# Performance work log

Measured on AMD Instinct MI355X. Metric: run time of the kernel, lower is better.

## Reference

```python
import jax, jax.numpy as jnp
import numpy as np

N = 100000   # nodes
E = 1600000  # edges (avg degree 16)
F = 128      # num_features
H = 128      # hidden_channels
C = 8        # num_classes


def _gcn_conv(x, src, dst, W, b, num_nodes):
    """PyG GCNConv: add self-loops, symmetric normalization, linear-then-aggregate, +bias."""
    h = x @ W  # [N, out]
    loops = jnp.arange(num_nodes, dtype=src.dtype)
    s = jnp.concatenate([src, loops])
    d = jnp.concatenate([dst, loops])
    deg = jax.ops.segment_sum(jnp.ones_like(s, dtype=h.dtype), d, num_segments=num_nodes)
    dinv = jax.lax.rsqrt(jnp.maximum(deg, 1.0))  # deg >= 1 thanks to self-loops
    norm = dinv[s] * dinv[d]  # [E+N]
    out = jax.ops.segment_sum(h[s] * norm[:, None], d, num_segments=num_nodes)
    return out + b


def setup_inputs() -> dict:
    key = jax.random.key(0)
    k1, k2, k3, k4 = jax.random.split(key, 4)
    x = jax.random.normal(k1, (N, F), dtype=jnp.float32)
    edge_index = jax.random.randint(k2, (2, E), 0, N, dtype=jnp.int32)
    W1 = jax.random.normal(k3, (F, H), dtype=jnp.float32) * (1.0 / np.sqrt(F))
    b1 = jnp.zeros((H,), dtype=jnp.float32)
    W2 = jax.random.normal(k4, (H, C), dtype=jnp.float32) * (1.0 / np.sqrt(H))
    b2 = jnp.zeros((C,), dtype=jnp.float32)
    return {"x": x, "edge_index": edge_index, "W1": W1, "b1": b1, "W2": W2, "b2": b2}


def reference(x, edge_index, W1, b1, W2, b2):
    src, dst = edge_index[0], edge_index[1]
    h = _gcn_conv(x, src, dst, W1, b1, N)
    h = jax.nn.relu(h)
    out = _gcn_conv(h, src, dst, W2, b2, N)
    return out
```

## Files before the change

kernel.cpp:

```cpp
#include <hip/hip_runtime.h>
#include <hip/hip_bf16.h>
#include <hip/hip_fp16.h>

#define NN 100000
#define EE 1600000
#define FF 128
#define HH 128
#define CC 8

#define CH 8192
#define NBK ((NN + 255) / 256)
#define NCH ((EE + CH - 1) / CH)
#define HSZ (NBK * NCH)
#define NT ((NN + 63) / 64)
#define G1B 320

typedef _Float16 half8 __attribute__((ext_vector_type(8)));
typedef float f32x4 __attribute__((ext_vector_type(4)));

__global__ __launch_bounds__(1024) void k_scan1(const int* __restrict__ in,
                                                int* __restrict__ outp,
                                                int* __restrict__ bsum, int n) {
  __shared__ int sh[1024];
  int t = threadIdx.x;
  int i = blockIdx.x * 1024 + t;
  int v = (i < n) ? in[i] : 0;
  sh[t] = v;
  __syncthreads();
  for (int offs = 1; offs < 1024; offs <<= 1) {
    int add = (t >= offs) ? sh[t - offs] : 0;
    __syncthreads();
    sh[t] += add;
    __syncthreads();
  }
  if (i < n) outp[i] = sh[t] - v;
  if (t == 1023) bsum[blockIdx.x] = sh[1023];
}

__global__ __launch_bounds__(256) void k_scan2(int* __restrict__ bsum, int nb) {
  __shared__ int sh[256];
  int t = threadIdx.x;
  int v = (t < nb) ? bsum[t] : 0;
  sh[t] = v;
  __syncthreads();
  for (int offs = 1; offs < 256; offs <<= 1) {
    int add = (t >= offs) ? sh[t - offs] : 0;
    __syncthreads();
    sh[t] += add;
    __syncthreads();
  }
  if (t < nb) bsum[t] = sh[t] - v;
}

__global__ __launch_bounds__(256) void k_histA(const int* __restrict__ dst,
                                               int* __restrict__ hist) {
  __shared__ int lh[NBK];
  int c = blockIdx.x, t = threadIdx.x;
  for (int b = t; b < NBK; b += 256) lh[b] = 0;
  __syncthreads();
  int e0 = c * CH, e1 = min(e0 + CH, EE);
  for (int j = e0 + t; j < e1; j += 256) atomicAdd(&lh[dst[j] >> 8], 1);
  __syncthreads();
  for (int b = t; b < NBK; b += 256) hist[b * NCH + c] = lh[b];
}

__global__ __launch_bounds__(256) void k_scat_gemm1(
    const int* __restrict__ src, const int* __restrict__ dst,
    const int* __restrict__ hist_s, const int* __restrict__ bsum,
    unsigned int* __restrict__ stage,
    const float* __restrict__ x, const float* __restrict__ W,
    __half* __restrict__ h, int n) {
  __shared__ _Float16 Wl[128 * 128];
  int t = threadIdx.x;

  if (blockIdx.x < NCH) {
    int* lcur = (int*)Wl;
    int c = blockIdx.x;
    for (int b = t; b < NBK; b += 256) {
      int idx = b * NCH + c;
      lcur[b] = hist_s[idx] + bsum[idx >> 10];
    }
    __syncthreads();
    int e0 = c * CH, e1 = min(e0 + CH, EE);
    for (int j = e0 + t; j < e1; j += 256) {
      int d = dst[j];
      int pos = atomicAdd(&lcur[d >> 8], 1);
      stage[pos] = (unsigned int)src[j] | ((unsigned int)(d & 255) << 17);
    }
    return;
  }

  {
    int c = t & 127;
    int kg0 = t >> 7;
    for (int kg = kg0; kg < 16; kg += 2) {
      _Float16 tmp[8];
#pragma unroll
      for (int j = 0; j < 8; ++j)
        tmp[j] = (_Float16)W[(size_t)(kg * 8 + j) * 128 + c];
      int byteoff = (c * 256 + kg * 16) ^ ((c & 7) << 4);
      *(half8*)((char*)Wl + byteoff) = *(half8*)tmp;
    }
  }
  __syncthreads();

  int w = t >> 6, l = t & 63;
  int rw = w >> 1, cw = w & 1;
  int lr = l & 15, g = l >> 4;

  for (int tile = blockIdx.x - NCH; tile < NT; tile += G1B) {
    int row0 = tile * 64;
    f32x4 acc[2][4];
#pragma unroll
    for (int ar = 0; ar < 2; ++ar)
#pragma unroll
      for (int bt = 0; bt < 4; ++bt)
#pragma unroll
        for (int r = 0; r < 4; ++r) acc[ar][bt][r] = 0.f;

    for (int kt = 0; kt < 4; ++kt) {
      half8 a[2];
#pragma unroll
      for (int ar = 0; ar < 2; ++ar) {
        int row = row0 + rw * 32 + ar * 16 + lr;
        if (row < n) {
          const float* p = &x[(size_t)row * 128 + kt * 32 + g * 8];
          float4 v0 = *(const float4*)p;
          float4 v1 = *(const float4*)(p + 4);
          a[ar][0] = (_Float16)v0.x; a[ar][1] = (_Float16)v0.y;
          a[ar][2] = (_Float16)v0.z; a[ar][3] = (_Float16)v0.w;
          a[ar][4] = (_Float16)v1.x; a[ar][5] = (_Float16)v1.y;
          a[ar][6] = (_Float16)v1.z; a[ar][7] = (_Float16)v1.w;
        } else {
#pragma unroll
          for (int j = 0; j < 8; ++j) a[ar][j] = (_Float16)0.f;
        }
      }
#pragma unroll
      for (int bt = 0; bt < 4; ++bt) {
        int c = cw * 64 + bt * 16 + lr;
        int byteoff = (c * 256 + kt * 64 + g * 16) ^ ((c & 7) << 4);
        half8 bb = *(const half8*)((const char*)Wl + byteoff);
        acc[0][bt] = __builtin_amdgcn_mfma_f32_16x16x32_f16(a[0], bb, acc[0][bt], 0, 0, 0);
        acc[1][bt] = __builtin_amdgcn_mfma_f32_16x16x32_f16(a[1], bb, acc[1][bt], 0, 0, 0);
      }
    }

#pragma unroll
    for (int ar = 0; ar < 2; ++ar)
#pragma unroll
      for (int bt = 0; bt < 4; ++bt)
#pragma unroll
        for (int r = 0; r < 4; ++r) {
          int row = row0 + rw * 32 + ar * 16 + g * 4 + r;
          int c = cw * 64 + bt * 16 + lr;
          if (row < n) h[(size_t)row * 128 + c] = __float2half(acc[ar][bt][r]);
        }
  }
}

__global__ __launch_bounds__(256) void k_bucketB(const unsigned int* __restrict__ stage,
                                                 const int* __restrict__ hist_s,
                                                 const int* __restrict__ bsum,
                                                 int* __restrict__ col,
                                                 int* __restrict__ rowptr,
                                                 float* __restrict__ dinv) {
  __shared__ int lcnt[256];
  __shared__ int lpart[256];
  int b = blockIdx.x, t = threadIdx.x;
  int n0 = b * 256;
  lcnt[t] = 0;
  int i0 = b * NCH;
  int e0 = hist_s[i0] + bsum[i0 >> 10];
  int e1;
  if (b == NBK - 1) {
    e1 = EE;
  } else {
    int i1 = (b + 1) * NCH;
    e1 = hist_s[i1] + bsum[i1 >> 10];
  }
  __syncthreads();
  for (int j = e0 + t; j < e1; j += 256)
    atomicAdd(&lcnt[stage[j] >> 17], 1);
  __syncthreads();
  int c = lcnt[t];
  lpart[t] = c;
  __syncthreads();
  for (int offs = 1; offs < 256; offs <<= 1) {
    int add = (t >= offs) ? lpart[t - offs] : 0;
    __syncthreads();
    lpart[t] += add;
    __syncthreads();
  }
  int base = e0 + lpart[t] - c;
  int node = n0 + t;
  if (node <= NN) rowptr[node] = base;
  if (node < NN) dinv[node] = rsqrtf((float)c + 1.f);
  __syncthreads();
  lcnt[t] = base;
  __syncthreads();
  for (int j = e0 + t; j < e1; j += 256) {
    unsigned int v = stage[j];
    int pos = atomicAdd(&lcnt[v >> 17], 1);
    col[pos] = (int)(v & 0x1FFFFu);
  }
}

__global__ __launch_bounds__(256) void k_agg1(const __half* __restrict__ h,
                                              const int* __restrict__ rowptr,
                                              const int* __restrict__ col,
                                              const float* __restrict__ dinv,
                                              const float* __restrict__ b1,
                                              __half2* __restrict__ out, int n) {
  int wid = threadIdx.x >> 6;
  int lane = threadIdx.x & 63;
  int node = blockIdx.x * 4 + wid;
  if (node >= n) return;
  float dn = dinv[node];
  const __half2* hp = (const __half2*)h;
  float2 acc = make_float2(0.f, 0.f);
  int e0 = rowptr[node], e1 = rowptr[node + 1];
  int e = e0;
  for (; e + 7 < e1; e += 8) {
    int s[8];
#pragma unroll
    for (int u = 0; u < 8; ++u) s[u] = col[e + u];
    float w[8];
    __half2 f[8];
#pragma unroll
    for (int u = 0; u < 8; ++u) w[u] = dinv[s[u]];
#pragma unroll
    for (int u = 0; u < 8; ++u) f[u] = hp[(size_t)s[u] * 64 + lane];
#pragma unroll
    for (int u = 0; u < 8; ++u) {
      float2 ff = __half22float2(f[u]);
      float ww = w[u] * dn;
      acc.x = fmaf(ww, ff.x, acc.x);
      acc.y = fmaf(ww, ff.y, acc.y);
    }
  }
  for (; e + 1 < e1; e += 2) {
    int s0 = col[e], s1 = col[e + 1];
    float w0 = dinv[s0] * dn, w1 = dinv[s1] * dn;
    float2 f0 = __half22float2(hp[(size_t)s0 * 64 + lane]);
    float2 f1 = __half22float2(hp[(size_t)s1 * 64 + lane]);
    acc.x = fmaf(w0, f0.x, acc.x); acc.y = fmaf(w0, f0.y, acc.y);
    acc.x = fmaf(w1, f1.x, acc.x); acc.y = fmaf(w1, f1.y, acc.y);
  }
  if (e < e1) {
    int s = col[e];
    float w = dinv[s] * dn;
    float2 f = __half22float2(hp[(size_t)s * 64 + lane]);
    acc.x = fmaf(w, f.x, acc.x);
    acc.y = fmaf(w, f.y, acc.y);
  }
  {
    float w = dn * dn;
    float2 f = __half22float2(hp[(size_t)node * 64 + lane]);
    acc.x = fmaf(w, f.x, acc.x);
    acc.y = fmaf(w, f.y, acc.y);
  }
  float2 bb = ((const float2*)b1)[lane];
  acc.x = fmaxf(acc.x + bb.x, 0.f);
  acc.y = fmaxf(acc.y + bb.y, 0.f);
  out[(size_t)node * 64 + lane] = __floats2half2_rn(acc.x, acc.y);
}

__global__ __launch_bounds__(256) void k_gemm2(const __half* __restrict__ a,
                                               const float* __restrict__ W2,
                                               __half* __restrict__ h2, int n) {
  int r = blockIdx.x * 256 + threadIdx.x;
  if (r >= n) return;
  float acc[8];
#pragma unroll
  for (int c = 0; c < 8; ++c) acc[c] = 0.f;
  const __half2* ap = (const __half2*)(a + (size_t)r * 128);
#pragma unroll 8
  for (int k2 = 0; k2 < 64; ++k2) {
    float2 v = __half22float2(ap[k2]);
    int k = k2 * 2;
#pragma unroll
    for (int c = 0; c < 8; ++c) {
      acc[c] = fmaf(v.x, W2[(k + 0) * 8 + c], acc[c]);
      acc[c] = fmaf(v.y, W2[(k + 1) * 8 + c], acc[c]);
    }
  }
  union { __half2 h2v[4]; uint4 u; } pk;
#pragma unroll
  for (int c = 0; c < 4; ++c)
    pk.h2v[c] = __floats2half2_rn(acc[2 * c], acc[2 * c + 1]);
  *(uint4*)&h2[(size_t)r * 8] = pk.u;
}

__global__ __launch_bounds__(256) void k_agg2(const __half* __restrict__ h2,
                                              const int* __restrict__ rowptr,
                                              const int* __restrict__ col,
                                              const float* __restrict__ dinv,
                                              const float* __restrict__ b2,
                                              float* __restrict__ out, int n) {
  int gthread = blockIdx.x * 256 + threadIdx.x;
  int node = gthread >> 3, f = gthread & 7;
  if (node >= n) return;
  float dn = dinv[node];
  float acc = 0.f;
  int e0 = rowptr[node], e1 = rowptr[node + 1];
  int e = e0;
  for (; e + 7 < e1; e += 8) {
    int s[8];
#pragma unroll
    for (int u = 0; u < 8; ++u) s[u] = col[e + u];
    float w[8];
    float v[8];
#pragma unroll
    for (int u = 0; u < 8; ++u) w[u] = dinv[s[u]];
#pragma unroll
    for (int u = 0; u < 8; ++u) v[u] = __half2float(h2[(size_t)s[u] * 8 + f]);
#pragma unroll
    for (int u = 0; u < 8; ++u) acc = fmaf(w[u] * dn, v[u], acc);
  }
  for (; e < e1; ++e) {
    int s = col[e];
    acc = fmaf(dinv[s] * dn, __half2float(h2[(size_t)s * 8 + f]), acc);
  }
  acc = fmaf(dn * dn, __half2float(h2[(size_t)node * 8 + f]), acc);
  out[(size_t)node * 8 + f] = acc + b2[f];
}

extern "C" void kernel_launch(void* const* d_in, const int* in_sizes, int n_in,
                              void* d_out, int out_size, void* d_ws, size_t ws_size,
                              hipStream_t stream) {
  const float* x  = (const float*)d_in[0];
  const int* eidx = (const int*)d_in[1];
  const float* W1 = (const float*)d_in[2];
  const float* b1 = (const float*)d_in[3];
  const float* W2 = (const float*)d_in[4];
  const float* b2 = (const float*)d_in[5];
  float* out = (float*)d_out;
  const int* src = eidx;
  const int* dst = eidx + EE;

  char* ws = (char*)d_ws;
  size_t off = 0;
  auto alloc = [&](size_t bytes) -> char* {
    char* p = ws + off;
    off = (off + bytes + 255) & ~(size_t)255;
    return p;
  };

  float*        dinv   = (float*)       alloc((size_t)NN * 4);
  int*          rowptr = (int*)         alloc((size_t)(NN + 1) * 4);
  int*          bsum   = (int*)         alloc(1024 * 4);
  int*          hist_g = (int*)         alloc((size_t)HSZ * 4);
  int*          hist_s = (int*)         alloc((size_t)HSZ * 4);
  unsigned int* stage  = (unsigned int*)alloc((size_t)EE * 4);
  int*          colbuf = (int*)         alloc((size_t)EE * 4);
  __half*       h1     = (__half*)      alloc((size_t)NN * HH * 2);
  __half2*      agg1   = (__half2*)     alloc((size_t)NN * HH * 2);
  __half*       h2     = (__half*)h1;

  int nbScanH = (HSZ + 1023) / 1024;

  k_histA<<<NCH, 256, 0, stream>>>(dst, hist_g);
  k_scan1<<<nbScanH, 1024, 0, stream>>>(hist_g, hist_s, bsum, HSZ);
  k_scan2<<<1, 256, 0, stream>>>(bsum, nbScanH);

  k_scat_gemm1<<<NCH + G1B, 256, 0, stream>>>(src, dst, hist_s, bsum, stage,
                                              x, W1, h1, NN);
  k_bucketB<<<NBK, 256, 0, stream>>>(stage, hist_s, bsum, colbuf, rowptr, dinv);

  k_agg1<<<(NN + 3) / 4, 256, 0, stream>>>(h1, rowptr, colbuf, dinv, b1, agg1, NN);
  k_gemm2<<<(NN + 255) / 256, 256, 0, stream>>>((const __half*)agg1, W2, h2, NN);
  k_agg2<<<(NN * 8 + 255) / 256, 256, 0, stream>>>(h2, rowptr, colbuf, dinv,
                                                   b2, out, NN);
}
```

Measured before the change: 169.5 us.

## Split GEMM1 across histogram and scatter kernels; fold bsum scan into consumers

The first 640 GEMM1 row tiles now run in the same launch as the destination histogram, and the remaining tiles run alongside the scatter pass, with one tile per block instead of a grid-stride loop. The separate single-block bsum scan kernel is removed: each scatter and bucket block rescans the small bsum array in LDS and turns it into an exclusive prefix. The aim is to cut one launch and fill idle CUs during the latency-bound histogram and scatter phases. In exchange every scatter and bucket block repeats a small redundant scan with extra barriers, and W1 is staged into LDS once per tile-block rather than once per persistent block.

```diff
diff --git a/kernel.cpp b/kernel.cpp
--- a/kernel.cpp
+++ b/kernel.cpp
@@ -12,11 +12,105 @@
 #define NBK ((NN + 255) / 256)
 #define NCH ((EE + CH - 1) / CH)
 #define HSZ (NBK * NCH)
+#define NSCAN ((HSZ + 1023) / 1024)
 #define NT ((NN + 63) / 64)
-#define G1B 320
+#define T1 640
 
 typedef _Float16 half8 __attribute__((ext_vector_type(8)));
 typedef float f32x4 __attribute__((ext_vector_type(4)));
+
+__device__ __forceinline__ void gemm1_tile(const float* __restrict__ x,
+                                           const _Float16* Wl,
+                                           __half* __restrict__ h, int n,
+                                           int tile, int t) {
+  int row0 = tile * 64;
+  int w = t >> 6, l = t & 63;
+  int rw = w >> 1, cw = w & 1;
+  int lr = l & 15, g = l >> 4;
+
+  f32x4 acc[2][4];
+#pragma unroll
+  for (int ar = 0; ar < 2; ++ar)
+#pragma unroll
+    for (int bt = 0; bt < 4; ++bt)
+#pragma unroll
+      for (int r = 0; r < 4; ++r) acc[ar][bt][r] = 0.f;
+
+  for (int kt = 0; kt < 4; ++kt) {
+    half8 a[2];
+#pragma unroll
+    for (int ar = 0; ar < 2; ++ar) {
+      int row = row0 + rw * 32 + ar * 16 + lr;
+      if (row < n) {
+        const float* p = &x[(size_t)row * 128 + kt * 32 + g * 8];
+        float4 v0 = *(const float4*)p;
+        float4 v1 = *(const float4*)(p + 4);
+        a[ar][0] = (_Float16)v0.x; a[ar][1] = (_Float16)v0.y;
+        a[ar][2] = (_Float16)v0.z; a[ar][3] = (_Float16)v0.w;
+        a[ar][4] = (_Float16)v1.x; a[ar][5] = (_Float16)v1.y;
+        a[ar][6] = (_Float16)v1.z; a[ar][7] = (_Float16)v1.w;
+      } else {
+#pragma unroll
+        for (int j = 0; j < 8; ++j) a[ar][j] = (_Float16)0.f;
+      }
+    }
+#pragma unroll
+    for (int bt = 0; bt < 4; ++bt) {
+      int c = cw * 64 + bt * 16 + lr;
+      int byteoff = (c * 256 + kt * 64 + g * 16) ^ ((c & 7) << 4);
+      half8 bb = *(const half8*)((const char*)Wl + byteoff);
+      acc[0][bt] = __builtin_amdgcn_mfma_f32_16x16x32_f16(a[0], bb, acc[0][bt], 0, 0, 0);
+      acc[1][bt] = __builtin_amdgcn_mfma_f32_16x16x32_f16(a[1], bb, acc[1][bt], 0, 0, 0);
+    }
+  }
+
+#pragma unroll
+  for (int ar = 0; ar < 2; ++ar)
+#pragma unroll
+    for (int bt = 0; bt < 4; ++bt)
+#pragma unroll
+      for (int r = 0; r < 4; ++r) {
+        int row = row0 + rw * 32 + ar * 16 + g * 4 + r;
+        int c = cw * 64 + bt * 16 + lr;
+        if (row < n) h[(size_t)row * 128 + c] = __float2half(acc[ar][bt][r]);
+      }
+}
+
+__device__ __forceinline__ void stage_W1(const float* __restrict__ W,
+                                         _Float16* Wl, int t) {
+  int c = t & 127;
+  int kg0 = t >> 7;
+  for (int kg = kg0; kg < 16; kg += 2) {
+    _Float16 tmp[8];
+#pragma unroll
+    for (int j = 0; j < 8; ++j)
+      tmp[j] = (_Float16)W[(size_t)(kg * 8 + j) * 128 + c];
+    int byteoff = (c * 256 + kg * 16) ^ ((c & 7) << 4);
+    *(half8*)((char*)Wl + byteoff) = *(half8*)tmp;
+  }
+}
+
+__global__ __launch_bounds__(256) void k_hist_g1(
+    const int* __restrict__ dst, int* __restrict__ hist,
+    const float* __restrict__ x, const float* __restrict__ W,
+    __half* __restrict__ h, int n) {
+  __shared__ _Float16 Wl[128 * 128];
+  int t = threadIdx.x;
+  if (blockIdx.x < NCH) {
+    int* lh = (int*)Wl;
+    int c = blockIdx.x;
+    for (int b = t; b < NBK; b += 256) lh[b] = 0;
+    __syncthreads();
+    int e0 = c * CH, e1 = min(e0 + CH, EE);
+    for (int j = e0 + t; j < e1; j += 256) atomicAdd(&lh[dst[j] >> 8], 1);
+    __syncthreads();
+    for (int b = t; b < NBK; b += 256) hist[b * NCH + c] = lh[b];
+    return;
+  }
+  stage_W1(W, Wl, t);
+  __syncthreads();
+  gemm1_tile(x, Wl, h, n, blockIdx.x - NCH, t);
+}
 
 __global__ __launch_bounds__(1024) void k_scan1(const int* __restrict__ in,
                                                 int* __restrict__ outp,
@@ -37,48 +131,36 @@
   if (t == 1023) bsum[blockIdx.x] = sh[1023];
 }
 
-__global__ __launch_bounds__(256) void k_scan2(int* __restrict__ bsum, int nb) {
-  __shared__ int sh[256];
-  int t = threadIdx.x;
-  int v = (t < nb) ? bsum[t] : 0;
-  sh[t] = v;
-  __syncthreads();
-  for (int offs = 1; offs < 256; offs <<= 1) {
-    int add = (t >= offs) ? sh[t - offs] : 0;
-    __syncthreads();
-    sh[t] += add;
-    __syncthreads();
-  }
-  if (t < nb) bsum[t] = sh[t] - v;
-}
-
-__global__ __launch_bounds__(256) void k_histA(const int* __restrict__ dst,
-                                               int* __restrict__ hist) {
-  __shared__ int lh[NBK];
-  int c = blockIdx.x, t = threadIdx.x;
-  for (int b = t; b < NBK; b += 256) lh[b] = 0;
-  __syncthreads();
-  int e0 = c * CH, e1 = min(e0 + CH, EE);
-  for (int j = e0 + t; j < e1; j += 256) atomicAdd(&lh[dst[j] >> 8], 1);
-  __syncthreads();
-  for (int b = t; b < NBK; b += 256) hist[b * NCH + c] = lh[b];
-}
-
-__global__ __launch_bounds__(256) void k_scat_gemm1(
+__device__ __forceinline__ void scan_bsum_lds(const int* __restrict__ bsum,
+                                              int* lbs, int t) {
+  if (t < 128) lbs[t] = (t < NSCAN) ? bsum[t] : 0;
+  __syncthreads();
+  for (int offs = 1; offs < 128; offs <<= 1) {
+    int add = (t >= offs && t < 128) ? lbs[t - offs] : 0;
+    __syncthreads();
+    if (t < 128) lbs[t] += add;
+    __syncthreads();
+  }
+}
+
+__global__ __launch_bounds__(256) void k_scat_g1(
     const int* __restrict__ src, const int* __restrict__ dst,
     const int* __restrict__ hist_s, const int* __restrict__ bsum,
     unsigned int* __restrict__ stage,
     const float* __restrict__ x, const float* __restrict__ W,
     __half* __restrict__ h, int n) {
   __shared__ _Float16 Wl[128 * 128];
+  __shared__ int lbs[128];
   int t = threadIdx.x;
 
   if (blockIdx.x < NCH) {
+    scan_bsum_lds(bsum, lbs, t);
     int* lcur = (int*)Wl;
     int c = blockIdx.x;
     for (int b = t; b < NBK; b += 256) {
       int idx = b * NCH + c;
-      lcur[b] = hist_s[idx] + bsum[idx >> 10];
+      int k = idx >> 10;
+      lcur[b] = hist_s[idx] + (k ? lbs[k - 1] : 0);
     }
     __syncthreads();
     int e0 = c * CH, e1 = min(e0 + CH, EE);
@@ -89,74 +171,9 @@
     }
     return;
   }
-
-  {
-    int c = t & 127;
-    int kg0 = t >> 7;
-    for (int kg = kg0; kg < 16; kg += 2) {
-      _Float16 tmp[8];
-#pragma unroll
-      for (int j = 0; j < 8; ++j)
-        tmp[j] = (_Float16)W[(size_t)(kg * 8 + j) * 128 + c];
-      int byteoff = (c * 256 + kg * 16) ^ ((c & 7) << 4);
-      *(half8*)((char*)Wl + byteoff) = *(half8*)tmp;
-    }
-  }
-  __syncthreads();
-
-  int w = t >> 6, l = t & 63;
-  int rw = w >> 1, cw = w & 1;
-  int lr = l & 15, g = l >> 4;
-
-  for (int tile = blockIdx.x - NCH; tile < NT; tile += G1B) {
-    int row0 = tile * 64;
-    f32x4 acc[2][4];
-#pragma unroll
-    for (int ar = 0; ar < 2; ++ar)
-#pragma unroll
-      for (int bt = 0; bt < 4; ++bt)
-#pragma unroll
-        for (int r = 0; r < 4; ++r) acc[ar][bt][r] = 0.f;
-
-    for (int kt = 0; kt < 4; ++kt) {
-      half8 a[2];
-#pragma unroll
-      for (int ar = 0; ar < 2; ++ar) {
-        int row = row0 + rw * 32 + ar * 16 + lr;
-        if (row < n) {
-          const float* p = &x[(size_t)row * 128 + kt * 32 + g * 8];
-          float4 v0 = *(const float4*)p;
-          float4 v1 = *(const float4*)(p + 4);
-          a[ar][0] = (_Float16)v0.x; a[ar][1] = (_Float16)v0.y;
-          a[ar][2] = (_Float16)v0.z; a[ar][3] = (_Float16)v0.w;
-          a[ar][4] = (_Float16)v1.x; a[ar][5] = (_Float16)v1.y;
-          a[ar][6] = (_Float16)v1.z; a[ar][7] = (_Float16)v1.w;
-        } else {
-#pragma unroll
-          for (int j = 0; j < 8; ++j) a[ar][j] = (_Float16)0.f;
-        }
-      }
-#pragma unroll
-      for (int bt = 0; bt < 4; ++bt) {
-        int c = cw * 64 + bt * 16 + lr;
-        int byteoff = (c * 256 + kt * 64 + g * 16) ^ ((c & 7) << 4);
-        half8 bb = *(const half8*)((const char*)Wl + byteoff);
-        acc[0][bt] = __builtin_amdgcn_mfma_f32_16x16x32_f16(a[0], bb, acc[0][bt], 0, 0, 0);
-        acc[1][bt] = __builtin_amdgcn_mfma_f32_16x16x32_f16(a[1], bb, acc[1][bt], 0, 0, 0);
-      }
-    }
-
-#pragma unroll
-    for (int ar = 0; ar < 2; ++ar)
-#pragma unroll
-      for (int bt = 0; bt < 4; ++bt)
-#pragma unroll
-        for (int r = 0; r < 4; ++r) {
-          int row = row0 + rw * 32 + ar * 16 + g * 4 + r;
-          int c = cw * 64 + bt * 16 + lr;
-          if (row < n) h[(size_t)row * 128 + c] = __float2half(acc[ar][bt][r]);
-        }
-  }
+  stage_W1(W, Wl, t);
+  __syncthreads();
+  gemm1_tile(x, Wl, h, n, T1 + blockIdx.x - NCH, t);
 }
 
 __global__ __launch_bounds__(256) void k_bucketB(const unsigned int* __restrict__ stage,
@@ -167,17 +184,21 @@
                                                  float* __restrict__ dinv) {
   __shared__ int lcnt[256];
   __shared__ int lpart[256];
+  __shared__ int lbs[128];
   int b = blockIdx.x, t = threadIdx.x;
   int n0 = b * 256;
   lcnt[t] = 0;
+  scan_bsum_lds(bsum, lbs, t);
   int i0 = b * NCH;
-  int e0 = hist_s[i0] + bsum[i0 >> 10];
+  int k0 = i0 >> 10;
+  int e0 = hist_s[i0] + (k0 ? lbs[k0 - 1] : 0);
   int e1;
   if (b == NBK - 1) {
     e1 = EE;
   } else {
     int i1 = (b + 1) * NCH;
-    e1 = hist_s[i1] + bsum[i1 >> 10];
+    int k1 = i1 >> 10;
+    e1 = hist_s[i1] + (k1 ? lbs[k1 - 1] : 0);
   }
   __syncthreads();
   for (int j = e0 + t; j < e1; j += 256)
@@ -358,14 +379,10 @@
   __half2*      agg1   = (__half2*)     alloc((size_t)NN * HH * 2);
   __half*       h2     = (__half*)h1;
 
-  int nbScanH = (HSZ + 1023) / 1024;
-
-  k_histA<<<NCH, 256, 0, stream>>>(dst, hist_g);
-  k_scan1<<<nbScanH, 1024, 0, stream>>>(hist_g, hist_s, bsum, HSZ);
-  k_scan2<<<1, 256, 0, stream>>>(bsum, nbScanH);
-
-  k_scat_gemm1<<<NCH + G1B, 256, 0, stream>>>(src, dst, hist_s, bsum, stage,
-                                              x, W1, h1, NN);
+  k_hist_g1<<<NCH + T1, 256, 0, stream>>>(dst, hist_g, x, W1, h1, NN);
+  k_scan1<<<NSCAN, 1024, 0, stream>>>(hist_g, hist_s, bsum, HSZ);
+  k_scat_g1<<<NCH + (NT - T1), 256, 0, stream>>>(src, dst, hist_s, bsum, stage,
+                                                 x, W1, h1, NN);
   k_bucketB<<<NBK, 256, 0, stream>>>(stage, hist_s, bsum, colbuf, rowptr, dinv);
 
   k_agg1<<<(NN + 3) / 4, 256, 0, stream>>>(h1, rowptr, colbuf, dinv, b1, agg1, NN);
```

Result: no change. 169.3 us (-0.1%).
